# Performance work log

Hardware: AMD Instinct MI355X
Metric: run time of the kernel (lower is better)

The kernel has to match this reference:

```python
import jax, jax.numpy as jnp
import numpy as np

H = 32  # hidden size
I = 1   # input size


def setup_inputs() -> dict:
    key = jax.random.key(0)
    ks = jax.random.split(key, 8)
    B, T = 1024, 2048
    s = 1.0 / np.sqrt(H)  # PyTorch default uniform init bound
    u = lambda k, shape: jax.random.uniform(k, shape, jnp.float32, -s, s)
    return {
        "x": jax.random.normal(ks[0], (B, T, I), jnp.float32),
        "W_ih": u(ks[1], (4 * H, I)),   # gate order: i, f, g, o
        "W_hh": u(ks[2], (4 * H, H)),
        "b_ih": u(ks[3], (4 * H,)),
        "b_hh": u(ks[4], (4 * H,)),
        "W_out": u(ks[5], (1, H)),
        "b_out": u(ks[6], (1,)),
    }


def reference(x, W_ih, W_hh, b_ih, b_hh, W_out, b_out):
    B, T, _ = x.shape
    # Precompute input contributions to all gates for all timesteps: [B,T,4H]
    xg = jnp.einsum('bti,gi->btg', x, W_ih) + b_ih + b_hh

    def step(carry, xg_t):
        h, c = carry  # each [B,H]
        gates = xg_t + h @ W_hh.T  # [B,4H]
        i, f, g, o = jnp.split(gates, 4, axis=-1)
        i = jax.nn.sigmoid(i)
        f = jax.nn.sigmoid(f)
        g = jnp.tanh(g)
        o = jax.nn.sigmoid(o)
        c = f * c + i * g
        h = o * jnp.tanh(c)
        return (h, c), h

    h0 = jnp.zeros((B, H), x.dtype)
    c0 = jnp.zeros((B, H), x.dtype)
    _, hs = jax.lax.scan(step, (h0, c0), jnp.swapaxes(xg, 0, 1))  # hs: [T,B,H]
    r_out = jnp.swapaxes(hs, 0, 1)  # [B,T,H]
    # Per-timestep linear (the original Python loop) == one batched matmul
    return jnp.einsum('bth,oh->bto', r_out, W_out) + b_out  # [B,T,1]
```

## Files before the change

kernel.cpp:

```cpp
#include <hip/hip_runtime.h>

#define LOG2E 1.44269504088896340736f

typedef _Float16 half2_t __attribute__((ext_vector_type(2)));

__device__ __forceinline__ float rlf(float v, int lane) {
    return __int_as_float(__builtin_amdgcn_readlane(__float_as_int(v), lane));
}
__device__ __forceinline__ unsigned rlu(unsigned v, int lane) {
    return (unsigned)__builtin_amdgcn_readlane((int)v, lane);
}
__device__ __forceinline__ unsigned pack2(float a, float b) {
    half2_t v; v.x = (_Float16)a; v.y = (_Float16)b;
    return __builtin_bit_cast(unsigned, v);
}
__device__ __forceinline__ half2_t ubc(unsigned u) {
    return __builtin_bit_cast(half2_t, u);
}

__device__ __forceinline__ float swap_half(float v) {
#if __has_builtin(__builtin_amdgcn_permlane32_swap)
    const unsigned u = __builtin_bit_cast(unsigned, v);
    auto r = __builtin_amdgcn_permlane32_swap(u, u, false, false);
    return __builtin_bit_cast(float, (unsigned)(r[0] ^ r[1] ^ u));
#else
    return __shfl_xor(v, 32, 64);
#endif
}

__device__ __forceinline__ float xor1_dpp(float v) {
    return __int_as_float(__builtin_amdgcn_mov_dpp(
        __float_as_int(v), 0xB1, 0xF, 0xF, true));
}

__global__ __launch_bounds__(64, 1) void lstm_pl_kernel(
    const float* __restrict__ x,
    const float* __restrict__ W_ih,
    const float* __restrict__ W_hh,
    const float* __restrict__ b_ih,
    const float* __restrict__ b_hh,
    const float* __restrict__ W_out,
    const float* __restrict__ b_out,
    float* __restrict__ out,
    int T)
{
    __shared__ float psum[64 * 68];
    __shared__ __align__(16) unsigned hbc[80];
    const int b = blockIdx.x;
    const int l = threadIdx.x;
    const int r0 = l;
    const int r1 = l + 64;
    const bool lo = (l < 32);

    const float sc0 = -LOG2E;
    const float sc1 = lo ? (-2.0f * LOG2E) : (-LOG2E);

    unsigned w0u[16], w1u[16];
#pragma unroll
    for (int m = 0; m < 16; ++m) {
        w0u[m] = pack2(W_hh[r0 * 32 + 2 * m] * sc0,
                       W_hh[r0 * 32 + 2 * m + 1] * sc0);
        w1u[m] = pack2(W_hh[r1 * 32 + 2 * m] * sc1,
                       W_hh[r1 * 32 + 2 * m + 1] * sc1);
    }
#pragma unroll
    for (int m = 0; m < 16; ++m)
        asm volatile("" : "+v"(w0u[m]), "+v"(w1u[m]));

    float4 wout4[8];
#pragma unroll
    for (int m = 0; m < 8; ++m)
        wout4[m] = *(const float4*)(W_out + 4 * m);

    const float wih0  = W_ih[r0] * sc0;
    const float wih1  = W_ih[r1] * sc1;
    const float bias0 = (b_ih[r0] + b_hh[r0]) * sc0;
    const float bias1 = (b_ih[r1] + b_hh[r1]) * sc1;
    const float A1s = lo ? (-4.0f * LOG2E) : 1.0f;
    const float B1s = lo ? ( 2.0f * LOG2E) : 0.0f;
    const float bout  = b_out[0];

    _Float16* hb16 = (_Float16*)hbc;
    const bool pub16 = lo && (l >= 8);
    const int waddr16 = pub16 ? l : (80 + l);

    float h = 0.0f, cs = 0.0f;
    unsigned hpk = 0u;
    uint4 hqB = {0,0,0,0}, hqC = {0,0,0,0}, hqD = {0,0,0,0};

    const float* xp = x + (size_t)b * T;
    float*       op = out + (size_t)b * T;
    float xv = xp[l];

    const uint4* hb4 = (const uint4*)hbc;

    for (int t0 = 0; t0 < T; t0 += 64) {
        const int tn = (t0 + 64 < T) ? (t0 + 64) : t0;
        float xv_next = xp[tn + l];

#pragma unroll 16
        for (int tu = 0; tu < 64; ++tu) {
            const float xt = rlf(xv, tu);

            const unsigned hp0 = rlu(hpk, 0);
            const unsigned hp1 = rlu(hpk, 2);
            const unsigned hp2 = rlu(hpk, 4);
            const unsigned hp3 = rlu(hpk, 6);

            float a0 = fmaf(wih0, xt, bias0);
            float a1 = fmaf(wih1, xt, bias1);
            float b0 = 0.0f, b1 = 0.0f;
            float c0 = 0.0f, c1 = 0.0f, d0 = 0.0f, d1 = 0.0f;

#define FD(acc, w, hh) acc = __builtin_amdgcn_fdot2(ubc(w), ubc(hh), acc, false)
            FD(c0, w0u[8],  hqC.x);  FD(d0, w0u[9],  hqC.y);
            FD(c1, w1u[8],  hqC.x);  FD(d1, w1u[9],  hqC.y);
            FD(c0, w0u[10], hqC.z);  FD(d0, w0u[11], hqC.w);
            FD(c1, w1u[10], hqC.z);  FD(d1, w1u[11], hqC.w);
            FD(c0, w0u[12], hqD.x);  FD(d0, w0u[13], hqD.y);
            FD(c1, w1u[12], hqD.x);  FD(d1, w1u[13], hqD.y);
            FD(c0, w0u[14], hqD.z);  FD(d0, w0u[15], hqD.w);
            FD(c1, w1u[14], hqD.z);  FD(d1, w1u[15], hqD.w);
            FD(a0, w0u[0],  hp0);    FD(b0, w0u[1],  hp1);
            FD(a1, w1u[0],  hp0);    FD(b1, w1u[1],  hp1);
            FD(a0, w0u[2],  hp2);    FD(b0, w0u[3],  hp3);
            FD(a1, w1u[2],  hp2);    FD(b1, w1u[3],  hp3);
            FD(a0, w0u[4],  hqB.x);  FD(b0, w0u[5],  hqB.y);
            FD(a1, w1u[4],  hqB.x);  FD(b1, w1u[5],  hqB.y);
            FD(a0, w0u[6],  hqB.z);  FD(b0, w0u[7],  hqB.w);
            FD(a1, w1u[6],  hqB.z);  FD(b1, w1u[7],  hqB.w);
#undef FD
            const float G0 = (a0 + b0) + (c0 + d0);
            const float G1 = (a1 + b1) + (c1 + d1);

            const float s0  = __builtin_amdgcn_rcpf(1.0f + __builtin_amdgcn_exp2f(G0));
            const float s1s = fmaf(A1s, __builtin_amdgcn_rcpf(
                                  1.0f + __builtin_amdgcn_exp2f(G1)), B1s);
            const float ig = s0 * s1s;

            const float o0 = swap_half(s0);
            const float o1 = swap_half(s1s);
            const float to1 = o1 + o1;

            cs = fmaf(o0, cs, ig);
            const float rc = __builtin_amdgcn_rcpf(
                1.0f + __builtin_amdgcn_exp2f(cs));
            h = fmaf(to1, rc, -o1);

            hb16[waddr16] = (_Float16)h;
            hqB = hb4[1];
            hqC = hb4[2];
            hqD = hb4[3];
            psum[tu * 68 + l] = h;

            const float hn = xor1_dpp(h);
            hpk = __builtin_bit_cast(unsigned,
                      __builtin_amdgcn_cvt_pkrtz(h, hn));
        }

        __syncthreads();
        const float4* row = (const float4*)(psum + l * 68);
        float4 s4;
        {
            float4 v4 = row[0];
            s4.x = v4.x * wout4[0].x; s4.y = v4.y * wout4[0].y;
            s4.z = v4.z * wout4[0].z; s4.w = v4.w * wout4[0].w;
        }
#pragma unroll
        for (int m = 1; m < 8; ++m) {
            float4 v4 = row[m];
            s4.x = fmaf(v4.x, wout4[m].x, s4.x);
            s4.y = fmaf(v4.y, wout4[m].y, s4.y);
            s4.z = fmaf(v4.z, wout4[m].z, s4.z);
            s4.w = fmaf(v4.w, wout4[m].w, s4.w);
        }
        op[t0 + l] = (s4.x + s4.y) + (s4.z + s4.w) + bout;
        __syncthreads();
        xv = xv_next;
    }
}

extern "C" void kernel_launch(void* const* d_in, const int* in_sizes, int n_in,
                              void* d_out, int out_size, void* d_ws, size_t ws_size,
                              hipStream_t stream) {
    const float* x     = (const float*)d_in[0];
    const float* W_ih  = (const float*)d_in[1];
    const float* W_hh  = (const float*)d_in[2];
    const float* b_ih  = (const float*)d_in[3];
    const float* b_hh  = (const float*)d_in[4];
    const float* W_out = (const float*)d_in[5];
    const float* b_out = (const float*)d_in[6];
    float* out = (float*)d_out;

    const int B = 1024;
    const int T = 2048;
    lstm_pl_kernel<<<B, 64, 0, stream>>>(x, W_ih, W_hh, b_ih, b_hh,
                                         W_out, b_out, out, T);
}
```

Before: 450.8 us.

## Broadcast hidden state via readlane only, dropping LDS round-trip per step

Replaces the per-step LDS publish/reload of the fp16 hidden vector with sixteen readlanes from the upper half-wave, so the recurrent state is broadcast entirely through scalar registers. Cell and hidden state now live in the upper 32 lanes, so only one swap_half is needed per step instead of two. The four split accumulators are folded into a single dependent fdot2 chain per gate row. This removes the LDS write/read latency from the serial recurrence, at the cost of more readlane instructions and a longer dependent dot-product chain.

```diff
diff --git a/kernel.cpp b/kernel.cpp
--- a/kernel.cpp
+++ b/kernel.cpp
@@ -45,7 +45,7 @@
     int T)
 {
     __shared__ float psum[64 * 68];
-    __shared__ __align__(16) unsigned hbc[80];
+
     const int b = blockIdx.x;
     const int l = threadIdx.x;
     const int r0 = l;
@@ -80,19 +80,14 @@
     const float B1s = lo ? ( 2.0f * LOG2E) : 0.0f;
     const float bout  = b_out[0];
 
-    _Float16* hb16 = (_Float16*)hbc;
-    const bool pub16 = lo && (l >= 8);
-    const int waddr16 = pub16 ? l : (80 + l);
+    const int pcol = lo ? (36 + l) : (l - 32);
 
     float h = 0.0f, cs = 0.0f;
     unsigned hpk = 0u;
-    uint4 hqB = {0,0,0,0}, hqC = {0,0,0,0}, hqD = {0,0,0,0};
 
     const float* xp = x + (size_t)b * T;
     float*       op = out + (size_t)b * T;
     float xv = xp[l];
-
-    const uint4* hb4 = (const uint4*)hbc;
 
     for (int t0 = 0; t0 < T; t0 += 64) {
         const int tn = (t0 + 64 < T) ? (t0 + 64) : t0;
@@ -102,60 +97,62 @@
         for (int tu = 0; tu < 64; ++tu) {
             const float xt = rlf(xv, tu);
 
-            const unsigned hp0 = rlu(hpk, 0);
-            const unsigned hp1 = rlu(hpk, 2);
-            const unsigned hp2 = rlu(hpk, 4);
-            const unsigned hp3 = rlu(hpk, 6);
+            const unsigned q0 = rlu(hpk, 32);
+            const unsigned q1 = rlu(hpk, 34);
+            const unsigned q2 = rlu(hpk, 36);
+            const unsigned q3 = rlu(hpk, 38);
 
             float a0 = fmaf(wih0, xt, bias0);
             float a1 = fmaf(wih1, xt, bias1);
-            float b0 = 0.0f, b1 = 0.0f;
-            float c0 = 0.0f, c1 = 0.0f, d0 = 0.0f, d1 = 0.0f;
 
 #define FD(acc, w, hh) acc = __builtin_amdgcn_fdot2(ubc(w), ubc(hh), acc, false)
-            FD(c0, w0u[8],  hqC.x);  FD(d0, w0u[9],  hqC.y);
-            FD(c1, w1u[8],  hqC.x);  FD(d1, w1u[9],  hqC.y);
-            FD(c0, w0u[10], hqC.z);  FD(d0, w0u[11], hqC.w);
-            FD(c1, w1u[10], hqC.z);  FD(d1, w1u[11], hqC.w);
-            FD(c0, w0u[12], hqD.x);  FD(d0, w0u[13], hqD.y);
-            FD(c1, w1u[12], hqD.x);  FD(d1, w1u[13], hqD.y);
-            FD(c0, w0u[14], hqD.z);  FD(d0, w0u[15], hqD.w);
-            FD(c1, w1u[14], hqD.z);  FD(d1, w1u[15], hqD.w);
-            FD(a0, w0u[0],  hp0);    FD(b0, w0u[1],  hp1);
-            FD(a1, w1u[0],  hp0);    FD(b1, w1u[1],  hp1);
-            FD(a0, w0u[2],  hp2);    FD(b0, w0u[3],  hp3);
-            FD(a1, w1u[2],  hp2);    FD(b1, w1u[3],  hp3);
-            FD(a0, w0u[4],  hqB.x);  FD(b0, w0u[5],  hqB.y);
-            FD(a1, w1u[4],  hqB.x);  FD(b1, w1u[5],  hqB.y);
-            FD(a0, w0u[6],  hqB.z);  FD(b0, w0u[7],  hqB.w);
-            FD(a1, w1u[6],  hqB.z);  FD(b1, w1u[7],  hqB.w);
+            FD(a0, w0u[0],  q0);  FD(a1, w1u[0],  q0);
+            FD(a0, w0u[1],  q1);  FD(a1, w1u[1],  q1);
+            const unsigned q4 = rlu(hpk, 40);
+            const unsigned q5 = rlu(hpk, 42);
+            const unsigned q6 = rlu(hpk, 44);
+            const unsigned q7 = rlu(hpk, 46);
+            FD(a0, w0u[2],  q2);  FD(a1, w1u[2],  q2);
+            FD(a0, w0u[3],  q3);  FD(a1, w1u[3],  q3);
+            const unsigned q8 = rlu(hpk, 48);
+            const unsigned q9 = rlu(hpk, 50);
+            const unsigned qA = rlu(hpk, 52);
+            const unsigned qB = rlu(hpk, 54);
+            FD(a0, w0u[4],  q4);  FD(a1, w1u[4],  q4);
+            FD(a0, w0u[5],  q5);  FD(a1, w1u[5],  q5);
+            const unsigned qC = rlu(hpk, 56);
+            const unsigned qD = rlu(hpk, 58);
+            const unsigned qE = rlu(hpk, 60);
+            const unsigned qF = rlu(hpk, 62);
+            FD(a0, w0u[6],  q6);  FD(a1, w1u[6],  q6);
+            FD(a0, w0u[7],  q7);  FD(a1, w1u[7],  q7);
+            FD(a0, w0u[8],  q8);  FD(a1, w1u[8],  q8);
+            FD(a0, w0u[9],  q9);  FD(a1, w1u[9],  q9);
+            FD(a0, w0u[10], qA);  FD(a1, w1u[10], qA);
+            FD(a0, w0u[11], qB);  FD(a1, w1u[11], qB);
+            FD(a0, w0u[12], qC);  FD(a1, w1u[12], qC);
+            FD(a0, w0u[13], qD);  FD(a1, w1u[13], qD);
+            FD(a0, w0u[14], qE);  FD(a1, w1u[14], qE);
+            FD(a0, w0u[15], qF);  FD(a1, w1u[15], qF);
 #undef FD
-            const float G0 = (a0 + b0) + (c0 + d0);
-            const float G1 = (a1 + b1) + (c1 + d1);
 
-            const float s0  = __builtin_amdgcn_rcpf(1.0f + __builtin_amdgcn_exp2f(G0));
+            const float s0  = __builtin_amdgcn_rcpf(1.0f + __builtin_amdgcn_exp2f(a0));
             const float s1s = fmaf(A1s, __builtin_amdgcn_rcpf(
-                                  1.0f + __builtin_amdgcn_exp2f(G1)), B1s);
-            const float ig = s0 * s1s;
+                                  1.0f + __builtin_amdgcn_exp2f(a1)), B1s);
 
-            const float o0 = swap_half(s0);
-            const float o1 = swap_half(s1s);
-            const float to1 = o1 + o1;
+            const float ig  = s0 * s1s;
+            const float igx = swap_half(ig);
 
-            cs = fmaf(o0, cs, ig);
+            cs = fmaf(s0, cs, igx);
             const float rc = __builtin_amdgcn_rcpf(
                 1.0f + __builtin_amdgcn_exp2f(cs));
-            h = fmaf(to1, rc, -o1);
-
-            hb16[waddr16] = (_Float16)h;
-            hqB = hb4[1];
-            hqC = hb4[2];
-            hqD = hb4[3];
-            psum[tu * 68 + l] = h;
+            const float ts = s1s + s1s;
+            h = fmaf(ts, rc, -s1s);
 
             const float hn = xor1_dpp(h);
             hpk = __builtin_bit_cast(unsigned,
                       __builtin_amdgcn_cvt_pkrtz(h, hn));
+            psum[tu * 68 + pcol] = h;
         }
 
         __syncthreads();
```

Result: faster. 388.7 us (-13.8%).
